# Performance work log

Measured on AMD Instinct MI355X. Metric: run time of the kernel, lower is better.

Reference implementation:

```python
import jax, jax.numpy as jnp
import numpy as np

N_HEADS = 16
ROPE_THETA = 10000.0


def _rope_cos_sin(T, head_dim, dtype):
    # freqs: (head_dim//2,), angles: (T, head_dim//2)
    freqs = 1.0 / ROPE_THETA ** (jnp.arange(0, head_dim, 2, dtype=jnp.float32) / head_dim)
    ang = jnp.arange(T, dtype=jnp.float32)[:, None] * freqs[None, :]
    return jnp.cos(ang).astype(dtype), jnp.sin(ang).astype(dtype)


def _apply_rope(x, cos, sin):
    # x: (B, H, T, D); cos/sin: (T, D//2)
    D = x.shape[-1]
    x1, x2 = x[..., : D // 2], x[..., D // 2 :]
    return jnp.concatenate([x1 * cos - x2 * sin, x1 * sin + x2 * cos], axis=-1)


def setup_inputs() -> dict:
    key = jax.random.key(0)
    ks = jax.random.split(key, 5)
    B, T, C = 2, 2048, 1024
    x = jax.random.normal(ks[0], (B, T, C), dtype=jnp.float32)
    w_attn = jax.random.normal(ks[1], (C, 3 * C), dtype=jnp.float32) * (C ** -0.5)
    b_attn = jax.random.normal(ks[2], (3 * C,), dtype=jnp.float32) * 0.02
    w_proj = jax.random.normal(ks[3], (C, C), dtype=jnp.float32) * (C ** -0.5)
    b_proj = jax.random.normal(ks[4], (C,), dtype=jnp.float32) * 0.02
    return {
        "x": x,
        "w_attn": w_attn,
        "b_attn": b_attn,
        "w_proj": w_proj,
        "b_proj": b_proj,
        "last_k_no_attend": 0,
        "window_size": 0,
    }


def reference(x, w_attn, b_attn, w_proj, b_proj, last_k_no_attend, window_size):
    B, T, C = x.shape
    H = N_HEADS
    D = C // H
    qkv = x @ w_attn + b_attn  # (B, T, 3C)
    q, k, v = jnp.split(qkv, 3, axis=-1)
    # (B, T, C) -> (B, H, T, D)
    to_heads = lambda t: t.reshape(B, T, H, D).transpose(0, 2, 1, 3)
    q, k, v = to_heads(q), to_heads(k), to_heads(v)
    cos, sin = _rope_cos_sin(T, D, x.dtype)
    q = _apply_rope(q, cos, sin)
    k = _apply_rope(k, cos, sin)
    scale = D ** -0.5
    attn = jnp.einsum("bhqd,bhkd->bhqk", q, k) * scale  # (B, H, T, T)
    causal = jnp.tril(jnp.ones((T, T), dtype=bool))
    attn = jnp.where(causal, attn, -jnp.inf)
    # last_k_no_attend/window_size default to 0 -> the custom-mask branch is
    # skipped (the nonzero branch in the source is ill-defined: it zeroes
    # entire rows producing NaN softmax).
    attn = jax.nn.softmax(attn, axis=-1)
    y = jnp.einsum("bhqk,bhkd->bhqd", attn, v)  # (B, H, T, D)
    y = y.transpose(0, 2, 1, 3).reshape(B, T, C)
    return y @ w_proj + b_proj
```

## Files before the change

### kernel.cpp

```cpp
#include <hip/hip_runtime.h>
#include <hip/hip_bf16.h>

typedef __bf16 bf16_t;
typedef __bf16 bf16x8 __attribute__((ext_vector_type(8)));
typedef float f32x4 __attribute__((ext_vector_type(4)));
typedef float f32x8v __attribute__((ext_vector_type(8)));

#define B_    2
#define T_    2048
#define C_    1024
#define H_    16
#define D_    64
#define M_    4096
#define NQKV_ 3072
#define PLD   72
#define NQT2  16
#define GTILE (128 * 64)
#define SLOT2 32768

static __device__ __forceinline__ float  bf2f(bf16_t x) { return (float)x; }
static __device__ __forceinline__ bf16_t f2bf(float x)  { return (bf16_t)x; }

typedef const __attribute__((address_space(1))) void gas_void;
typedef __attribute__((address_space(3))) void las_void;
static __device__ __forceinline__ void gld16(const void* g, void* l) {
  __builtin_amdgcn_global_load_lds((gas_void*)g, (las_void*)l, 16, 0, 0);
}

__global__ __launch_bounds__(256) void rope_tab_k(float2* __restrict__ tab) {
  int i = blockIdx.x * 256 + threadIdx.x;
  int tpos = i >> 5, d = i & 31;
  float fr = exp2f(-(float)d * (13.287712379549449f / 32.0f));
  float ang = (float)tpos * fr;
  tab[i] = make_float2(cosf(ang), sinf(ang));
}

__global__ __launch_bounds__(256) void f32_to_bf16_k(const float* __restrict__ in,
                                                     bf16_t* __restrict__ out) {
  const int i = (blockIdx.x * 256 + threadIdx.x) * 8;
  f32x8v v = *(const f32x8v*)(in + i);
  bf16x8 h;
#pragma unroll
  for (int j = 0; j < 8; ++j) h[j] = f2bf(v[j]);
  *(bf16x8*)(out + i) = h;
}

__global__ __launch_bounds__(256) void transpose_f32_bf16(const float* __restrict__ in,
                                                          bf16_t* __restrict__ out,
                                                          int R, int Ccols) {
  __shared__ bf16_t tile[32][33];
  int tx = threadIdx.x & 31, ty = threadIdx.x >> 5;
  int c0 = blockIdx.x * 32, r0 = blockIdx.y * 32;
#pragma unroll
  for (int j = 0; j < 4; ++j)
    tile[ty + j * 8][tx] = f2bf(in[(size_t)(r0 + ty + j * 8) * Ccols + c0 + tx]);
  __syncthreads();
#pragma unroll
  for (int j = 0; j < 4; ++j)
    out[(size_t)(c0 + ty + j * 8) * R + r0 + tx] = tile[tx][ty + j * 8];
}

__device__ __forceinline__ void gemm_core(const bf16_t* __restrict__ A,
                                          const bf16_t* __restrict__ Bt,
                                          int m0, int n0,
                                          bf16_t* sm,
                                          f32x4 acc[4][4]) {
  const int t    = threadIdx.x;
  const int lane = t & 63, w = t >> 6;
  const int wr = (w >> 1) * 64, wc = (w & 1) * 64;
  const int l15 = lane & 15, g4 = lane >> 4;

  const f32x4 z4 = {0.f, 0.f, 0.f, 0.f};
#pragma unroll
  for (int i = 0; i < 4; ++i)
#pragma unroll
    for (int j = 0; j < 4; ++j) acc[i][j] = z4;

  const int srow = w * 32 + (lane >> 3);
  const int sel8 = (lane & 7) * 8;
  const bf16_t* gA = A  + (size_t)(m0 + srow) * C_ + sel8;
  const bf16_t* gB = Bt + (size_t)(n0 + srow) * C_ + sel8;
  const int dOff = (w * 32) * 64;

#pragma unroll
  for (int j = 0; j < 4; ++j) {
    gld16(gA + (size_t)(j * 8) * C_, sm + dOff + j * 8 * 64);
    gld16(gB + (size_t)(j * 8) * C_, sm + GTILE + dOff + j * 8 * 64);
  }
  __syncthreads();

  int cur = 0;
  for (int kt = 0; kt < C_ / 64; ++kt) {
    if (kt + 1 < C_ / 64) {
      const int k0 = (kt + 1) * 64;
      bf16_t* nA = sm + (cur ^ 1) * (2 * GTILE);
      bf16_t* nB = nA + GTILE;
#pragma unroll
      for (int j = 0; j < 4; ++j) {
        gld16(gA + (size_t)(j * 8) * C_ + k0, nA + dOff + j * 8 * 64);
        gld16(gB + (size_t)(j * 8) * C_ + k0, nB + dOff + j * 8 * 64);
      }
    }
    const bf16_t* lA = sm + cur * (2 * GTILE);
    const bf16_t* lB = lA + GTILE;
#pragma unroll
    for (int ks = 0; ks < 2; ++ks) {
      bf16x8 af[4], bfv[4];
#pragma unroll
      for (int mi = 0; mi < 4; ++mi)
        af[mi] = *(const bf16x8*)&lA[(wr + mi * 16 + l15) * 64 + ks * 32 + g4 * 8];
#pragma unroll
      for (int ni = 0; ni < 4; ++ni)
        bfv[ni] = *(const bf16x8*)&lB[(wc + ni * 16 + l15) * 64 + ks * 32 + g4 * 8];
#pragma unroll
      for (int mi = 0; mi < 4; ++mi)
#pragma unroll
        for (int ni = 0; ni < 4; ++ni)
          acc[mi][ni] = __builtin_amdgcn_mfma_f32_16x16x32_bf16(af[mi], bfv[ni],
                                                                acc[mi][ni], 0, 0, 0);
    }
    __syncthreads();
    cur ^= 1;
  }
}

__global__ __launch_bounds__(512, 2) void qkv_gemm(const bf16_t* __restrict__ x,
                                                   const bf16_t* __restrict__ wT,
                                                   const float* __restrict__ bias,
                                                   const float2* __restrict__ rtab,
                                                   bf16_t* __restrict__ qo,
                                                   bf16_t* __restrict__ ko,
                                                   bf16_t* __restrict__ vo) {
  __shared__ __align__(16) bf16_t sm[2 * SLOT2];
  const int t = threadIdx.x;
  const int lane = t & 63, w = t >> 6;
  const int l15 = lane & 15, g4 = lane >> 4;
  const int wr = (w >> 2) * 128, wc = (w & 3) * 64;

  const int bid = blockIdx.x;
  const int swz = (bid & 7) * 24 + (bid >> 3);
  const int m0 = (swz & 15) * 256, n0 = (swz >> 4) * 256;

  const f32x4 z4 = {0.f, 0.f, 0.f, 0.f};
  f32x4 acc[8][4];
#pragma unroll
  for (int i = 0; i < 8; ++i)
#pragma unroll
    for (int j = 0; j < 4; ++j) acc[i][j] = z4;

  const int sr8 = lane >> 3;
  const int swc = ((lane & 7) ^ ((lane >> 3) & 7)) * 8;
  const bf16_t* gA = x  + (size_t)(m0 + w * 32 + sr8) * C_ + swc;
  const bf16_t* gB = wT + (size_t)(n0 + w * 32 + sr8) * C_ + swc;

#define QKV_STAGE(h)                                                            \
  {                                                                             \
    bf16_t* sl = sm + ((h) & 1) * SLOT2;                                        \
    const size_t kofs = (size_t)(h) * 64;                                       \
    gld16(gA + kofs,            sl + (w * 32 +  0) * 64);                       \
    gld16(gA +  8 * C_ + kofs,  sl + (w * 32 +  8) * 64);                       \
    gld16(gA + 16 * C_ + kofs,  sl + (w * 32 + 16) * 64);                       \
    gld16(gA + 24 * C_ + kofs,  sl + (w * 32 + 24) * 64);                       \
    gld16(gB + kofs,            sl + 16384 + (w * 32 +  0) * 64);               \
    gld16(gB +  8 * C_ + kofs,  sl + 16384 + (w * 32 +  8) * 64);               \
    gld16(gB + 16 * C_ + kofs,  sl + 16384 + (w * 32 + 16) * 64);               \
    gld16(gB + 24 * C_ + kofs,  sl + 16384 + (w * 32 + 24) * 64);               \
  }

  QKV_STAGE(0);

  const int csw = l15 & 7;

  for (int h = 0; h < 16; ++h) {
    asm volatile("s_waitcnt vmcnt(0)" ::: "memory");
    __builtin_amdgcn_sched_barrier(0);
    __builtin_amdgcn_s_barrier();
    __builtin_amdgcn_sched_barrier(0);
    if (h + 1 < 16) QKV_STAGE(h + 1);

    const bf16_t* sl = sm + (h & 1) * SLOT2;
#pragma unroll
    for (int ks = 0; ks < 2; ++ks) {
      bf16x8 af[8], bfv[4];
#pragma unroll
      for (int mi = 0; mi < 8; ++mi)
        af[mi] = *(const bf16x8*)&sl[(wr + mi * 16 + l15) * 64 + (((ks * 4 + g4) ^ csw) * 8)];
#pragma unroll
      for (int ni = 0; ni < 4; ++ni)
        bfv[ni] = *(const bf16x8*)&sl[16384 + (wc + ni * 16 + l15) * 64 + (((ks * 4 + g4) ^ csw) * 8)];
#pragma unroll
      for (int mi = 0; mi < 8; ++mi)
#pragma unroll
        for (int ni = 0; ni < 4; ++ni)
          acc[mi][ni] = __builtin_amdgcn_mfma_f32_16x16x32_bf16(af[mi], bfv[ni],
                                                                acc[mi][ni], 0, 0, 0);
    }
  }
#undef QKV_STAGE

  __syncthreads();
  bf16_t* stg = sm + w * 8192;

  const int ng  = n0 + wc;
  const int sel = ng >> 10;
  const int h2  = (ng & 1023) >> 6;

  if (sel < 2) {
    const float qs = (sel == 0) ? 0.125f * 1.4426950408889634f : 1.0f;
#pragma unroll
    for (int mi = 0; mi < 8; ++mi) {
#pragma unroll
      for (int ni = 0; ni < 2; ++ni) {
        const int d1 = ni * 16 + l15;
        const float b1 = bias[ng + d1];
        const float b2 = bias[ng + d1 + 32];
#pragma unroll
        for (int r = 0; r < 4; ++r) {
          const int lrow = mi * 16 + g4 * 4 + r;
          const int tpos = (m0 + wr + lrow) & (T_ - 1);
          const float2 cs = rtab[tpos * 32 + d1];
          const float x1 = acc[mi][ni][r]     + b1;
          const float x2 = acc[mi][ni + 2][r] + b2;
          stg[lrow * 64 + d1]      = f2bf((x1 * cs.x - x2 * cs.y) * qs);
          stg[lrow * 64 + d1 + 32] = f2bf((x1 * cs.y + x2 * cs.x) * qs);
        }
      }
    }
  } else {
#pragma unroll
    for (int mi = 0; mi < 8; ++mi)
#pragma unroll
      for (int ni = 0; ni < 4; ++ni) {
        const int d = ni * 16 + l15;
        const float b1 = bias[ng + d];
#pragma unroll
        for (int r = 0; r < 4; ++r)
          stg[(mi * 16 + g4 * 4 + r) * 64 + d] = f2bf(acc[mi][ni][r] + b1);
      }
  }

  bf16_t* outp = (sel == 0) ? qo : (sel == 1 ? ko : vo);
  const int a  = lane >> 3;
  const int b8 = (lane & 7) * 8;
#pragma unroll
  for (int p = 0; p < 16; ++p) {
    const int lrow = p * 8 + a;
    const int row  = m0 + wr + lrow;
    const int tpos = row & (T_ - 1);
    const int bb   = row >> 11;
    uint4 val = *(const uint4*)&stg[lrow * 64 + b8];
    *(uint4*)(outp + ((size_t)(bb * H_ + h2) * T_ + tpos) * D_ + b8) = val;
  }
}

__global__ __launch_bounds__(512) void attn_fwd(const bf16_t* __restrict__ q,
                                                const bf16_t* __restrict__ k,
                                                const bf16_t* __restrict__ v,
                                                bf16_t* __restrict__ y) {
  __shared__ __align__(16) bf16_t Ks[64 * 64];
  __shared__ __align__(16) bf16_t Vt[64 * PLD];
  const int t = threadIdx.x;
  const int lane = t & 63, w = t >> 6;
  const int l15 = lane & 15, g4 = lane >> 4;

  const int f   = blockIdx.x;
  const int idx = f & 255;
  const int bh  = idx & 31;
  const int p   = idx >> 5;
  const int qt  = (f >> 8) ? (15 - p) : p;
  const int qb  = qt * 128;
  const size_t hb = (size_t)bh * T_ * D_;

  const int qrow = qb + w * 16 + l15;
  bf16x8 qf[2];
  qf[0] = *(const bf16x8*)(q + hb + (size_t)qrow * D_ + g4 * 8);
  qf[1] = *(const bf16x8*)(q + hb + (size_t)qrow * D_ + 32 + g4 * 8);

  const f32x4 z4 = {0.f, 0.f, 0.f, 0.f};
  f32x4 o[4];
#pragma unroll
  for (int i = 0; i < 4; ++i) o[i] = z4;
  float mx = -1e30f, L = 0.f;

  const int skk = t >> 3;
  const int sd0 = (t & 7) * 8;
  const int u   = t & 7;
  const int ksw = sd0 ^ ((skk & 7) * 8);
  const int slot = ((skk >> 5) & 1) * 32 + ((skk >> 2) & 3) * 8 + ((skk >> 4) & 1) * 4 + (skk & 3);
  const int pos  = (((slot >> 3) ^ u) << 3) | (slot & 7);
  const int rowb = qb + w * 16 + g4 * 4;

  const int ntiles = 2 * qt + 2;

  uint4 kv = *(const uint4*)(k + hb + (size_t)skk * D_ + sd0);
  uint4 vv = *(const uint4*)(v + hb + (size_t)skk * D_ + sd0);

  for (int it = 0; it < ntiles; ++it) {
    const int kb = it * 64;
    __syncthreads();
    *(uint4*)&Ks[skk * 64 + ksw] = kv;
    {
      const bf16_t* vb = (const bf16_t*)&vv;
#pragma unroll
      for (int i = 0; i < 8; ++i)
        Vt[(sd0 + i) * PLD + pos] = vb[i];
    }
    __syncthreads();

    if (it + 1 < ntiles) {
      const size_t nb = hb + (size_t)(kb + 64 + skk) * D_ + sd0;
      kv = *(const uint4*)(k + nb);
      vv = *(const uint4*)(v + nb);
    }

    const bool last = (it == ntiles - 1);
    if (last && w < 4) continue;

    f32x4 s[4];
#pragma unroll
    for (int c = 0; c < 4; ++c) s[c] = z4;
#pragma unroll
    for (int ks = 0; ks < 2; ++ks)
#pragma unroll
      for (int c = 0; c < 4; ++c) {
        const int kr = c * 16 + l15;
        bf16x8 kf = *(const bf16x8*)&Ks[kr * 64 + ((ks * 32 + g4 * 8) ^ ((kr & 7) * 8))];
        s[c] = __builtin_amdgcn_mfma_f32_16x16x32_bf16(kf, qf[ks], s[c], 0, 0, 0);
      }

    if (last || (it == ntiles - 2 && w < 4)) {
#pragma unroll
      for (int c = 0; c < 4; ++c)
#pragma unroll
        for (int r = 0; r < 4; ++r)
          if (kb + c * 16 + g4 * 4 + r > qrow) s[c][r] = -1e30f;
    }

    float tm = -1e30f;
#pragma unroll
    for (int c = 0; c < 4; ++c)
#pragma unroll
      for (int r = 0; r < 4; ++r) tm = fmaxf(tm, s[c][r]);
    tm = fmaxf(tm, __shfl_xor(tm, 16));
    tm = fmaxf(tm, __shfl_xor(tm, 32));
    if (!__all(tm - mx <= 8.0f)) {
      const float mnew = fmaxf(mx, tm);
      const float sc = exp2f(mx - mnew);
      L *= sc;
      float scr[4];
#pragma unroll
      for (int r = 0; r < 4; ++r)
        scr[r] = __shfl(sc, (lane & 48) | (g4 * 4 + r));
#pragma unroll
      for (int nf = 0; nf < 4; ++nf)
#pragma unroll
        for (int r = 0; r < 4; ++r) o[nf][r] *= scr[r];
      mx = mnew;
    }
    float rs = 0.f;
#pragma unroll
    for (int c = 0; c < 4; ++c)
#pragma unroll
      for (int r = 0; r < 4; ++r) {
        s[c][r] = exp2f(s[c][r] - mx);
        rs += s[c][r];
      }
    rs += __shfl_xor(rs, 16);
    rs += __shfl_xor(rs, 32);
    L += rs;

    bf16x8 ap0, ap1;
#pragma unroll
    for (int r = 0; r < 4; ++r) {
      ap0[r]     = f2bf(s[0][r]);
      ap0[4 + r] = f2bf(s[1][r]);
      ap1[r]     = f2bf(s[2][r]);
      ap1[4 + r] = f2bf(s[3][r]);
    }

#pragma unroll
    for (int nf = 0; nf < 4; ++nf) {
      const int d  = nf * 16 + l15;
      const int h3 = (2 * nf + (l15 >> 3)) & 7;
      bf16x8 vf0 = *(const bf16x8*)&Vt[d * PLD + ((g4 ^ h3) << 3)];
      bf16x8 vf1 = *(const bf16x8*)&Vt[d * PLD + (((g4 + 4) ^ h3) << 3)];
      o[nf] = __builtin_amdgcn_mfma_f32_16x16x32_bf16(ap0, vf0, o[nf], 0, 0, 0);
      o[nf] = __builtin_amdgcn_mfma_f32_16x16x32_bf16(ap1, vf1, o[nf], 0, 0, 0);
    }
  }

  const int bb = bh / H_, hh = bh % H_;
  float il[4];
#pragma unroll
  for (int r = 0; r < 4; ++r)
    il[r] = 1.0f / __shfl(L, (lane & 48) | (g4 * 4 + r));
#pragma unroll
  for (int nf = 0; nf < 4; ++nf)
#pragma unroll
    for (int r = 0; r < 4; ++r) {
      const int row = rowb + r;
      y[(size_t)(bb * T_ + row) * C_ + hh * D_ + nf * 16 + l15] = f2bf(o[nf][r] * il[r]);
    }
}

__global__ __launch_bounds__(256) void proj_gemm(const bf16_t* __restrict__ yin,
                                                 const bf16_t* __restrict__ wT,
                                                 const float* __restrict__ bias,
                                                 float* __restrict__ out) {
  __shared__ __align__(16) bf16_t smem[4 * GTILE];
  f32x4 acc[4][4];
  const int bid = blockIdx.x;
  const int swz = (bid & 7) * 32 + (bid >> 3);
  const int m0 = (swz & 31) * 128, n0 = (swz >> 5) * 128;
  gemm_core(yin, wT, m0, n0, smem, acc);

  const int t = threadIdx.x;
  const int lane = t & 63, w = t >> 6;
  const int wr = (w >> 1) * 64, wc = (w & 1) * 64;
  const int l15 = lane & 15, g4 = lane >> 4;
  const int ng = n0 + wc;
#pragma unroll
  for (int mi = 0; mi < 4; ++mi) {
    const int rowb = m0 + wr + mi * 16 + g4 * 4;
#pragma unroll
    for (int ni = 0; ni < 4; ++ni) {
      const int n = ng + ni * 16 + l15;
      const float b1 = bias[n];
#pragma unroll
      for (int r = 0; r < 4; ++r)
        out[(size_t)(rowb + r) * C_ + n] = acc[mi][ni][r] + b1;
    }
  }
}

extern "C" void kernel_launch(void* const* d_in, const int* in_sizes, int n_in,
                              void* d_out, int out_size, void* d_ws, size_t ws_size,
                              hipStream_t stream) {
  (void)in_sizes; (void)n_in; (void)out_size; (void)ws_size;
  const float* x      = (const float*)d_in[0];
  const float* w_attn = (const float*)d_in[1];
  const float* b_attn = (const float*)d_in[2];
  const float* w_proj = (const float*)d_in[3];
  const float* b_proj = (const float*)d_in[4];
  float* out = (float*)d_out;

  char* ws = (char*)d_ws;
  bf16_t* wTa = (bf16_t*)ws;  ws += (size_t)NQKV_ * C_ * 2;
  bf16_t* wTp = (bf16_t*)ws;  ws += (size_t)C_ * C_ * 2;
  bf16_t* qb  = (bf16_t*)ws;  ws += (size_t)B_ * H_ * T_ * D_ * 2;
  bf16_t* kb  = (bf16_t*)ws;  ws += (size_t)B_ * H_ * T_ * D_ * 2;
  bf16_t* vb  = (bf16_t*)ws;  ws += (size_t)B_ * H_ * T_ * D_ * 2;
  bf16_t* yb  = (bf16_t*)ws;  ws += (size_t)B_ * T_ * C_ * 2;
  float2* rtab = (float2*)ws; ws += (size_t)T_ * 32 * sizeof(float2);
  bf16_t* x_bf = yb;

  rope_tab_k<<<dim3(T_ * 32 / 256), 256, 0, stream>>>(rtab);
  transpose_f32_bf16<<<dim3(NQKV_ / 32, C_ / 32), 256, 0, stream>>>(w_attn, wTa, C_, NQKV_);
  transpose_f32_bf16<<<dim3(C_ / 32,   C_ / 32), 256, 0, stream>>>(w_proj, wTp, C_, C_);
  f32_to_bf16_k<<<dim3(M_ * C_ / (256 * 8)), 256, 0, stream>>>(x, x_bf);
  qkv_gemm<<<dim3((M_ / 256) * (NQKV_ / 256)), 512, 0, stream>>>(x_bf, wTa, b_attn, rtab, qb, kb, vb);
  attn_fwd<<<dim3(NQT2 * 32), 512, 0, stream>>>(qb, kb, vb, yb);
  proj_gemm<<<dim3((M_ / 128) * (C_ / 128)), 256, 0, stream>>>(yb, wTp, b_proj, out);
}
```

Baseline: 115.7 us.

## Double-buffer K/V shared tiles in attention to drop one barrier per iteration

The attention kernel now keeps two LDS buffers for K and transposed V. Each iteration computes on the current buffer, writes the prefetched next tile into the other buffer, and then hits a single __syncthreads, where the old code needed two barriers per tile. This removes one barrier and lets the LDS stores overlap with other waves' compute, at the cost of doubling the shared memory footprint, which may reduce occupancy.

```diff
diff --git a/kernel.cpp b/kernel.cpp
--- a/kernel.cpp
+++ b/kernel.cpp
@@ -17,6 +17,8 @@
 #define NQT2  16
 #define GTILE (128 * 64)
 #define SLOT2 32768
+#define KSB   4096
+#define VTB   (64 * PLD)
 
 static __device__ __forceinline__ float  bf2f(bf16_t x) { return (float)x; }
 static __device__ __forceinline__ bf16_t f2bf(float x)  { return (bf16_t)x; }
@@ -257,8 +259,8 @@
                                                 const bf16_t* __restrict__ k,
                                                 const bf16_t* __restrict__ v,
                                                 bf16_t* __restrict__ y) {
-  __shared__ __align__(16) bf16_t Ks[64 * 64];
-  __shared__ __align__(16) bf16_t Vt[64 * PLD];
+  __shared__ __align__(16) bf16_t Ks[2 * KSB];
+  __shared__ __align__(16) bf16_t Vt[2 * VTB];
   const int t = threadIdx.x;
   const int lane = t & 63, w = t >> 6;
   const int l15 = lane & 15, g4 = lane >> 4;
@@ -292,20 +294,22 @@
 
   const int ntiles = 2 * qt + 2;
 
-  uint4 kv = *(const uint4*)(k + hb + (size_t)skk * D_ + sd0);
-  uint4 vv = *(const uint4*)(v + hb + (size_t)skk * D_ + sd0);
-
+  {
+    uint4 kv0 = *(const uint4*)(k + hb + (size_t)skk * D_ + sd0);
+    uint4 vv0 = *(const uint4*)(v + hb + (size_t)skk * D_ + sd0);
+    *(uint4*)&Ks[skk * 64 + ksw] = kv0;
+    const bf16_t* vb = (const bf16_t*)&vv0;
+#pragma unroll
+    for (int i = 0; i < 8; ++i)
+      Vt[(sd0 + i) * PLD + pos] = vb[i];
+  }
+  __syncthreads();
+
+  uint4 kv, vv;
   for (int it = 0; it < ntiles; ++it) {
-    const int kb = it * 64;
-    __syncthreads();
-    *(uint4*)&Ks[skk * 64 + ksw] = kv;
-    {
-      const bf16_t* vb = (const bf16_t*)&vv;
-#pragma unroll
-      for (int i = 0; i < 8; ++i)
-        Vt[(sd0 + i) * PLD + pos] = vb[i];
-    }
-    __syncthreads();
+    const int kb  = it * 64;
+    const int cur = it & 1;
+    const bool last = (it == ntiles - 1);
 
     if (it + 1 < ntiles) {
       const size_t nb = hb + (size_t)(kb + 64 + skk) * D_ + sd0;
@@ -313,80 +317,93 @@
       vv = *(const uint4*)(v + nb);
     }
 
-    const bool last = (it == ntiles - 1);
-    if (last && w < 4) continue;
-
-    f32x4 s[4];
-#pragma unroll
-    for (int c = 0; c < 4; ++c) s[c] = z4;
-#pragma unroll
-    for (int ks = 0; ks < 2; ++ks)
-#pragma unroll
-      for (int c = 0; c < 4; ++c) {
-        const int kr = c * 16 + l15;
-        bf16x8 kf = *(const bf16x8*)&Ks[kr * 64 + ((ks * 32 + g4 * 8) ^ ((kr & 7) * 8))];
-        s[c] = __builtin_amdgcn_mfma_f32_16x16x32_bf16(kf, qf[ks], s[c], 0, 0, 0);
-      }
-
-    if (last || (it == ntiles - 2 && w < 4)) {
+    if (!(last && w < 4)) {
+      const bf16_t* KsC = Ks + cur * KSB;
+      const bf16_t* VtC = Vt + cur * VTB;
+
+      f32x4 s[4];
+#pragma unroll
+      for (int c = 0; c < 4; ++c) s[c] = z4;
+#pragma unroll
+      for (int ks = 0; ks < 2; ++ks)
+#pragma unroll
+        for (int c = 0; c < 4; ++c) {
+          const int kr = c * 16 + l15;
+          bf16x8 kf = *(const bf16x8*)&KsC[kr * 64 + ((ks * 32 + g4 * 8) ^ ((kr & 7) * 8))];
+          s[c] = __builtin_amdgcn_mfma_f32_16x16x32_bf16(kf, qf[ks], s[c], 0, 0, 0);
+        }
+
+      if (last || (it == ntiles - 2 && w < 4)) {
+#pragma unroll
+        for (int c = 0; c < 4; ++c)
+#pragma unroll
+          for (int r = 0; r < 4; ++r)
+            if (kb + c * 16 + g4 * 4 + r > qrow) s[c][r] = -1e30f;
+      }
+
+      float tm = -1e30f;
 #pragma unroll
       for (int c = 0; c < 4; ++c)
 #pragma unroll
+        for (int r = 0; r < 4; ++r) tm = fmaxf(tm, s[c][r]);
+      tm = fmaxf(tm, __shfl_xor(tm, 16));
+      tm = fmaxf(tm, __shfl_xor(tm, 32));
+      if (!__all(tm - mx <= 8.0f)) {
+        const float mnew = fmaxf(mx, tm);
+        const float sc = exp2f(mx - mnew);
+        L *= sc;
+        float scr[4];
+#pragma unroll
         for (int r = 0; r < 4; ++r)
-          if (kb + c * 16 + g4 * 4 + r > qrow) s[c][r] = -1e30f;
-    }
-
-    float tm = -1e30f;
-#pragma unroll
-    for (int c = 0; c < 4; ++c)
-#pragma unroll
-      for (int r = 0; r < 4; ++r) tm = fmaxf(tm, s[c][r]);
-    tm = fmaxf(tm, __shfl_xor(tm, 16));
-    tm = fmaxf(tm, __shfl_xor(tm, 32));
-    if (!__all(tm - mx <= 8.0f)) {
-      const float mnew = fmaxf(mx, tm);
-      const float sc = exp2f(mx - mnew);
-      L *= sc;
-      float scr[4];
-#pragma unroll
-      for (int r = 0; r < 4; ++r)
-        scr[r] = __shfl(sc, (lane & 48) | (g4 * 4 + r));
-#pragma unroll
-      for (int nf = 0; nf < 4; ++nf)
-#pragma unroll
-        for (int r = 0; r < 4; ++r) o[nf][r] *= scr[r];
-      mx = mnew;
-    }
-    float rs = 0.f;
-#pragma unroll
-    for (int c = 0; c < 4; ++c)
+          scr[r] = __shfl(sc, (lane & 48) | (g4 * 4 + r));
+#pragma unroll
+        for (int nf = 0; nf < 4; ++nf)
+#pragma unroll
+          for (int r = 0; r < 4; ++r) o[nf][r] *= scr[r];
+        mx = mnew;
+      }
+      float rs = 0.f;
+#pragma unroll
+      for (int c = 0; c < 4; ++c)
+#pragma unroll
+        for (int r = 0; r < 4; ++r) {
+          s[c][r] = exp2f(s[c][r] - mx);
+          rs += s[c][r];
+        }
+      rs += __shfl_xor(rs, 16);
+      rs += __shfl_xor(rs, 32);
+      L += rs;
+
+      bf16x8 ap0, ap1;
 #pragma unroll
       for (int r = 0; r < 4; ++r) {
-        s[c][r] = exp2f(s[c][r] - mx);
-        rs += s[c][r];
-      }
-    rs += __shfl_xor(rs, 16);
-    rs += __shfl_xor(rs, 32);
-    L += rs;
-
-    bf16x8 ap0, ap1;
-#pragma unroll
-    for (int r = 0; r < 4; ++r) {
-      ap0[r]     = f2bf(s[0][r]);
-      ap0[4 + r] = f2bf(s[1][r]);
-      ap1[r]     = f2bf(s[2][r]);
-      ap1[4 + r] = f2bf(s[3][r]);
-    }
-
-#pragma unroll
-    for (int nf = 0; nf < 4; ++nf) {
-      const int d  = nf * 16 + l15;
-      const int h3 = (2 * nf + (l15 >> 3)) & 7;
-      bf16x8 vf0 = *(const bf16x8*)&Vt[d * PLD + ((g4 ^ h3) << 3)];
-      bf16x8 vf1 = *(const bf16x8*)&Vt[d * PLD + (((g4 + 4) ^ h3) << 3)];
-      o[nf] = __builtin_amdgcn_mfma_f32_16x16x32_bf16(ap0, vf0, o[nf], 0, 0, 0);
-      o[nf] = __builtin_amdgcn_mfma_f32_16x16x32_bf16(ap1, vf1, o[nf], 0, 0, 0);
-    }
+        ap0[r]     = f2bf(s[0][r]);
+        ap0[4 + r] = f2bf(s[1][r]);
+        ap1[r]     = f2bf(s[2][r]);
+        ap1[4 + r] = f2bf(s[3][r]);
+      }
+
+#pragma unroll
+      for (int nf = 0; nf < 4; ++nf) {
+        const int d  = nf * 16 + l15;
+        const int h3 = (2 * nf + (l15 >> 3)) & 7;
+        bf16x8 vf0 = *(const bf16x8*)&VtC[d * PLD + ((g4 ^ h3) << 3)];
+        bf16x8 vf1 = *(const bf16x8*)&VtC[d * PLD + (((g4 + 4) ^ h3) << 3)];
+        o[nf] = __builtin_amdgcn_mfma_f32_16x16x32_bf16(ap0, vf0, o[nf], 0, 0, 0);
+        o[nf] = __builtin_amdgcn_mfma_f32_16x16x32_bf16(ap1, vf1, o[nf], 0, 0, 0);
+      }
+    }
+
+    if (it + 1 < ntiles) {
+      bf16_t* KsN = Ks + (cur ^ 1) * KSB;
+      bf16_t* VtN = Vt + (cur ^ 1) * VTB;
+      *(uint4*)&KsN[skk * 64 + ksw] = kv;
+      const bf16_t* vb = (const bf16_t*)&vv;
+#pragma unroll
+      for (int i = 0; i < 8; ++i)
+        VtN[(sd0 + i) * PLD + pos] = vb[i];
+    }
+    __syncthreads();
   }
 
   const int bb = bh / H_, hh = bh % H_;
```

Result: no change. 115.4 us (-0.2%).
